# Kernel optimization log

Measured on AMD Instinct MI355X. Metric: run time of the kernel, lower is better.

The kernel has to match this reference:

```python
import jax, jax.numpy as jnp
import numpy as np

N_NODES = 50000
N_EDGES = 800000
IN_CH = 256
OUT_CH = 128


def setup_inputs() -> dict:
    key = jax.random.key(0)
    k1, k2, k3, k4, k5, k6 = jax.random.split(key, 6)
    x = jax.random.normal(k1, (N_NODES, IN_CH), dtype=jnp.float32)
    edge_rows = jax.random.randint(k2, (N_EDGES,), 0, N_NODES, dtype=jnp.int64)
    edge_cols = jax.random.randint(k3, (N_EDGES,), 0, N_NODES, dtype=jnp.int64)
    # positive edge weights, roughly like a normalized adjacency (~1/degree)
    edge_vals = jax.random.uniform(k4, (N_EDGES,), dtype=jnp.float32) / 16.0
    # xavier_uniform: bound = sqrt(6/(fan_in+fan_out))
    bound = float(np.sqrt(6.0 / (IN_CH + OUT_CH)))
    weight = jax.random.uniform(k5, (IN_CH, OUT_CH), dtype=jnp.float32, minval=-bound, maxval=bound)
    gate_weight = jax.random.uniform(k6, (IN_CH, OUT_CH), dtype=jnp.float32, minval=-bound, maxval=bound)
    return {"x": x, "edge_rows": edge_rows, "edge_cols": edge_cols,
            "edge_vals": edge_vals, "weight": weight, "gate_weight": gate_weight}


def _spmm(edge_rows, edge_cols, edge_vals, dense, n_rows):
    # out[r] = sum over edges (r, c, v): v * dense[c]
    gathered = edge_vals[:, None] * dense[edge_cols]  # [E, out_ch]
    return jax.ops.segment_sum(gathered, edge_rows, num_segments=n_rows)


def reference(x, edge_rows, edge_cols, edge_vals, weight, gate_weight):
    support = x @ weight          # [N, out_ch]
    gate = x @ gate_weight        # [N, out_ch]
    n = x.shape[0]
    agg_support = _spmm(edge_rows, edge_cols, edge_vals, support, n)
    agg_gate = _spmm(edge_rows, edge_cols, edge_vals, gate, n)
    return jax.nn.sigmoid(agg_gate) * agg_support
```

## Files before the change

### kernel.cpp

```cpp
#include <hip/hip_runtime.h>
#include <hip/hip_bf16.h>

#define IN_CH 256
#define OUT_CH 128
#define CAP 64
#define RPB 128
#define EPB 4096
#define NBIN 392
#define METAST 400

typedef __attribute__((ext_vector_type(8))) short bf16x8;
typedef __attribute__((ext_vector_type(4))) float f32x4;

__device__ __forceinline__ unsigned short f2bf(float f) {
  unsigned int u = __builtin_bit_cast(unsigned int, f);
  u += 0x7FFFu + ((u >> 16) & 1u);
  return (unsigned short)(u >> 16);
}
__device__ __forceinline__ unsigned int pack2bf(float a, float b) {
  return (unsigned int)f2bf(a) | ((unsigned int)f2bf(b) << 16);
}
__device__ __forceinline__ float bflo(unsigned int u) {
  return __builtin_bit_cast(float, u << 16);
}
__device__ __forceinline__ float bfhi(unsigned int u) {
  return __builtin_bit_cast(float, u & 0xFFFF0000u);
}

__global__ __launch_bounds__(256) void init_wcat(
    const float* __restrict__ w, const float* __restrict__ gw,
    unsigned short* __restrict__ wcat2) {
  const int c = blockIdx.x;
  const int k = threadIdx.x;
  const int wc = c >> 6, s = c & 63, n = s >> 4, lr = s & 15;
  const int ch = 32 * wc + (n & 1) * 16 + lr;
  const float v = (n < 2) ? w[(size_t)k * 128 + ch]
                          : gw[(size_t)k * 128 + ch];
  wcat2[(size_t)c * 256 + k] = f2bf(v);
}

#define AST 80

__global__ __launch_bounds__(256) void gemm_and_bin(
    const float* __restrict__ x, const unsigned short* __restrict__ wcat2,
    char* __restrict__ comb, int nrows,
    const int* __restrict__ er, const int* __restrict__ ec,
    const float* __restrict__ ev, uint2* __restrict__ seg,
    unsigned* __restrict__ meta, int E, int binBlocks) {
  __shared__ char smem[37728];

  if (blockIdx.x < binBlocks) {
    uint2* image = (uint2*)smem;
    int* hist = (int*)(smem + 32768);
    int* offs = (int*)(smem + 32768 + 1568);
    int* cur  = (int*)(smem + 32768 + 3136);
    int* gsum = (int*)(smem + 32768 + 4704);
    const int t = threadIdx.x;
    const int e0 = blockIdx.x * EPB;

    for (int j = t; j < NBIN; j += 256) hist[j] = 0;
    __syncthreads();

    int myr[16];
#pragma unroll
    for (int i = 0; i < 16; ++i) {
      const int e = e0 + i * 256 + t;
      int r = -1;
      if (e < E) { r = er[e]; atomicAdd(&hist[r >> 7], 1); }
      myr[i] = r;
    }
    __syncthreads();

    if (t < 49) {
      int s = 0;
#pragma unroll
      for (int k2 = 0; k2 < 8; ++k2) {
        const int j = t * 8 + k2;
        if (j < NBIN) { cur[j] = s; s += hist[j]; }
      }
      gsum[t] = s;
    }
    __syncthreads();
    if (t == 0) {
      int s = 0;
      for (int b2 = 0; b2 < 49; ++b2) { const int g = gsum[b2]; gsum[b2] = s; s += g; }
    }
    __syncthreads();
    if (t < 49) {
#pragma unroll
      for (int k2 = 0; k2 < 8; ++k2) {
        const int j = t * 8 + k2;
        if (j < NBIN) offs[j] = cur[j] + gsum[t];
      }
    }
    __syncthreads();
    for (int j = t; j < NBIN; j += 256) cur[j] = offs[j];
    __syncthreads();

#pragma unroll
    for (int i = 0; i < 16; ++i) {
      const int r = myr[i];
      if (r >= 0) {
        const int e = e0 + i * 256 + t;
        const int b2 = r >> 7;
        const int idx = atomicAdd(&cur[b2], 1);
        image[idx] = make_uint2(((unsigned)ec[e] << 16) | (unsigned)f2bf(ev[e]),
                                (unsigned)(r & (RPB - 1)));
      }
    }
    __syncthreads();

    uint2* segb = seg + (size_t)blockIdx.x * EPB;
    for (int s2 = t; s2 < EPB; s2 += 256) segb[s2] = image[s2];
    unsigned* metab = meta + (size_t)blockIdx.x * METAST;
    for (int j = t; j < NBIN - 1; j += 256)
      metab[j] = (unsigned)offs[j] | ((unsigned)hist[j] << 16);
    return;
  }

  char* As = smem;
  char* Bs = smem + 64 * AST;
  const int t = threadIdx.x;
  const int lane = t & 63;
  const int wc = t >> 6;
  const int lrow = lane & 15;
  const int klane = lane >> 4;
  const int blockRow = (blockIdx.x - binBlocks) * 64;

  f32x4 acc[4][4];
#pragma unroll
  for (int m = 0; m < 4; ++m)
#pragma unroll
    for (int n = 0; n < 4; ++n) acc[m][n] = (f32x4){0.f, 0.f, 0.f, 0.f};

  const int arow = t >> 2;
  const int aseg = t & 3;
  const int agrow = blockRow + arow;
  const bool aok = (agrow < nrows);
  const float* xrow = x + (size_t)agrow * IN_CH + aseg * 8;
  const char* bsrc0 = (const char*)wcat2 + (size_t)t * 512;

  for (int kt = 0; kt < IN_CH; kt += 32) {
    {
      float4 v0 = make_float4(0, 0, 0, 0), v1 = v0;
      if (aok) {
        v0 = *(const float4*)(xrow + kt);
        v1 = *(const float4*)(xrow + kt + 4);
      }
      uint4 pk;
      pk.x = pack2bf(v0.x, v0.y); pk.y = pack2bf(v0.z, v0.w);
      pk.z = pack2bf(v1.x, v1.y); pk.w = pack2bf(v1.z, v1.w);
      *(uint4*)(As + arow * AST + aseg * 16) = pk;
    }
    {
      const char* src = bsrc0 + kt * 2;
      char* dst = Bs + t * AST;
      *(uint4*)(dst + 0)  = *(const uint4*)(src + 0);
      *(uint4*)(dst + 16) = *(const uint4*)(src + 16);
      *(uint4*)(dst + 32) = *(const uint4*)(src + 32);
      *(uint4*)(dst + 48) = *(const uint4*)(src + 48);
    }
    __syncthreads();

    bf16x8 af[4], bfm[4];
#pragma unroll
    for (int m = 0; m < 4; ++m)
      af[m] = *(const bf16x8*)(As + (m * 16 + lrow) * AST + klane * 16);
#pragma unroll
    for (int n = 0; n < 4; ++n)
      bfm[n] = *(const bf16x8*)(Bs + (wc * 64 + n * 16 + lrow) * AST + klane * 16);
#pragma unroll
    for (int m = 0; m < 4; ++m)
#pragma unroll
      for (int n = 0; n < 4; ++n)
        acc[m][n] = __builtin_amdgcn_mfma_f32_16x16x32_bf16(af[m], bfm[n], acc[m][n], 0, 0, 0);
    __syncthreads();
  }

#pragma unroll
  for (int m = 0; m < 4; ++m) {
#pragma unroll
    for (int j = 0; j < 4; ++j) {
      const int grow = blockRow + m * 16 + klane * 4 + j;
      if (grow < nrows) {
        uint2 val;
        val.x = pack2bf(acc[m][0][j], acc[m][2][j]);
        val.y = pack2bf(acc[m][1][j], acc[m][3][j]);
        *(uint2*)(comb + (size_t)grow * 512 + wc * 128 + lrow * 8) = val;
      }
    }
  }
}

__global__ __launch_bounds__(256) void bin_fine2(
    const uint2* __restrict__ seg, const unsigned* __restrict__ meta,
    int* __restrict__ cnt, unsigned* __restrict__ bucket4,
    int nrows, int nblk) {
  __shared__ unsigned fine[RPB * CAP];
  __shared__ int lcnt[RPB];
  __shared__ int roff[224];
  __shared__ int S[224];
  __shared__ int Pex[225];
  const int t = threadIdx.x;
  const int j = blockIdx.x;
  const int r0 = j * RPB;

  for (int k = t; k < RPB; k += 256) lcnt[k] = 0;
  if (t < 224) {
    if (t < nblk) {
      const unsigned m = meta[(size_t)t * METAST + j];
      roff[t] = (int)(m & 0xFFFFu);
      S[t] = (int)(m >> 16);
    } else {
      S[t] = 0;
    }
  }
  __syncthreads();

  for (int d = 1; d < 224; d <<= 1) {
    int v = 0;
    if (t < 224 && t >= d) v = S[t - d];
    __syncthreads();
    if (t < 224) S[t] += v;
    __syncthreads();
  }
  if (t == 0) Pex[0] = 0;
  if (t < 224) Pex[t + 1] = S[t];
  __syncthreads();

  const int nE = Pex[nblk];
  for (int e = t; e < nE; e += 256) {
    int lo = 0, hi = nblk - 1;
    while (lo < hi) {
      const int mid = (lo + hi + 1) >> 1;
      if (Pex[mid] <= e) lo = mid; else hi = mid - 1;
    }
    const int i = e - Pex[lo];
    const uint2 ent = seg[(size_t)lo * EPB + roff[lo] + i];
    const int rl = (int)ent.y;
    const int idx = atomicAdd(&lcnt[rl], 1);
    if (idx < CAP) fine[rl * CAP + idx] = ent.x;
  }
  __syncthreads();

  if (t < RPB && r0 + t < nrows) cnt[r0 + t] = min(lcnt[t], CAP);

  for (int s = t; s < RPB * CAP; s += 256) {
    const int rl = s >> 6;
    const int sl = s & 63;
    if (sl < min(lcnt[rl], CAP) && r0 + rl < nrows)
      bucket4[(size_t)(r0 + rl) * CAP + sl] = fine[s];
  }
}

__global__ __launch_bounds__(256) void spmm_fused(
    const unsigned* __restrict__ bucket4, const int* __restrict__ cnt,
    const char* __restrict__ comb, float* __restrict__ out, int nrows) {
  const int wid = (int)((blockIdx.x * 256 + threadIdx.x) >> 6);
  const int lane = threadIdx.x & 63;
  if (wid >= nrows) return;

  const int deg = min(cnt[wid], CAP);
  float s1 = 0.f, g1 = 0.f, s2 = 0.f, g2 = 0.f;

  if (deg > 0) {
    const unsigned my = bucket4[(size_t)wid * CAP + lane];
    for (int d = 0; d < deg; d += 8) {
      unsigned cj[8]; float vj[8]; uint2 q[8];
#pragma unroll
      for (int j = 0; j < 8; ++j) {
        const int dj = d + j;
        const int ds = dj < deg ? dj : deg - 1;
        const unsigned ent = (unsigned)__shfl((int)my, ds);
        cj[j] = ent >> 16;
        vj[j] = (dj < deg) ? bflo(ent) : 0.f;
      }
#pragma unroll
      for (int j = 0; j < 8; ++j)
        q[j] = *(const uint2*)(comb + (size_t)cj[j] * 512 + lane * 8);
#pragma unroll
      for (int j = 0; j < 8; ++j) {
        s1 += vj[j] * bflo(q[j].x);  g1 += vj[j] * bfhi(q[j].x);
        s2 += vj[j] * bflo(q[j].y);  g2 += vj[j] * bfhi(q[j].y);
      }
    }
  }
  const int gg = lane >> 4, lr = lane & 15;
  const int c1 = 32 * gg + lr;
  const float o1 = s1 / (1.f + __expf(-g1));
  const float o2 = s2 / (1.f + __expf(-g2));
  out[(size_t)wid * OUT_CH + c1]      = o1;
  out[(size_t)wid * OUT_CH + c1 + 16] = o2;
}

extern "C" void kernel_launch(void* const* d_in, const int* in_sizes, int n_in,
                              void* d_out, int out_size, void* d_ws, size_t ws_size,
                              hipStream_t stream) {
  const float* x  = (const float*)d_in[0];
  const int*   er = (const int*)d_in[1];
  const int*   ec = (const int*)d_in[2];
  const float* ev = (const float*)d_in[3];
  const float* w  = (const float*)d_in[4];
  const float* gw = (const float*)d_in[5];
  float* out = (float*)d_out;

  const int N = in_sizes[0] / IN_CH;
  const int E = in_sizes[1];
  const int nbins = (N + RPB - 1) / RPB;
  const int binBlocks = (E + EPB - 1) / EPB;

  char* ws = (char*)d_ws;
  char* comb = ws;
  size_t off = (size_t)N * 512;
  unsigned short* wcat2 = (unsigned short*)(ws + off);  off += 256 * 256 * 2;
  int* cnt = (int*)(ws + off);                          off += ((size_t)N * 4 + 255) & ~255ull;
  unsigned* bucket4 = (unsigned*)(ws + off);            off += (size_t)N * CAP * 4;
  uint2* seg = (uint2*)(ws + off);                      off += (size_t)binBlocks * EPB * 8;
  unsigned* meta = (unsigned*)(ws + off);

  init_wcat<<<256, 256, 0, stream>>>(w, gw, wcat2);

  const int gemmBlocks = (N + 63) / 64;
  gemm_and_bin<<<binBlocks + gemmBlocks, 256, 0, stream>>>(
      x, wcat2, comb, N, er, ec, ev, seg, meta, E, binBlocks);

  bin_fine2<<<nbins, 256, 0, stream>>>(seg, meta, cnt, bucket4, N, binBlocks);

  const int blocks = (N + 3) / 4;
  spmm_fused<<<blocks, 256, 0, stream>>>(bucket4, cnt, comb, out, N);
}
```

Baseline: 105.3 us.

## Split x conversion from GEMM, fuse GEMM with fine binning, use LDS direct loads

A new first kernel converts x to bf16 in place inside the workspace while the coarse binning runs alongside it. The GEMM then moves into a 512-thread kernel that stages tiles with global_load_lds and shares its launch with the fine-binning blocks, so the old separate bin_fine2 launch is gone. The GEMM also writes its output over the bf16 x buffer it reads from. Coarse-bin entries are split into a 4-byte column/value array and a 1-byte row array to cut traffic, and the SpMM gather batch grows from 8 to 16 loads. Costs are an extra full pass over x in bf16 and a hazard: a GEMM block overwrites rows of combx that other blocks may still be reading, although each block reads only its own 128 rows.

```diff
diff --git a/kernel.cpp b/kernel.cpp
--- a/kernel.cpp
+++ b/kernel.cpp
@@ -25,6 +25,12 @@
 }
 __device__ __forceinline__ float bfhi(unsigned int u) {
   return __builtin_bit_cast(float, u & 0xFFFF0000u);
+}
+
+__device__ __forceinline__ void gl16(const void* g, void* l) {
+  __builtin_amdgcn_global_load_lds(
+      (const __attribute__((address_space(1))) void*)g,
+      (__attribute__((address_space(3))) void*)l, 16, 0, 0);
 }
 
 __global__ __launch_bounds__(256) void init_wcat(
@@ -39,173 +45,193 @@
   wcat2[(size_t)c * 256 + k] = f2bf(v);
 }
 
-#define AST 80
-
-__global__ __launch_bounds__(256) void gemm_and_bin(
-    const float* __restrict__ x, const unsigned short* __restrict__ wcat2,
-    char* __restrict__ comb, int nrows,
+__global__ __launch_bounds__(256) void cvt_and_bin(
+    const float* __restrict__ x, char* __restrict__ combx, int out16max,
     const int* __restrict__ er, const int* __restrict__ ec,
-    const float* __restrict__ ev, uint2* __restrict__ seg,
-    unsigned* __restrict__ meta, int E, int binBlocks) {
+    const float* __restrict__ ev, unsigned* __restrict__ cA,
+    unsigned* __restrict__ cB32, unsigned* __restrict__ meta,
+    int E, int nbins, int cvtBlocks) {
   __shared__ char smem[37728];
-
-  if (blockIdx.x < binBlocks) {
-    uint2* image = (uint2*)smem;
-    int* hist = (int*)(smem + 32768);
-    int* offs = (int*)(smem + 32768 + 1568);
-    int* cur  = (int*)(smem + 32768 + 3136);
-    int* gsum = (int*)(smem + 32768 + 4704);
-    const int t = threadIdx.x;
-    const int e0 = blockIdx.x * EPB;
-
-    for (int j = t; j < NBIN; j += 256) hist[j] = 0;
-    __syncthreads();
-
-    int myr[16];
-#pragma unroll
-    for (int i = 0; i < 16; ++i) {
+  const int t = threadIdx.x;
+
+  if ((int)blockIdx.x < cvtBlocks) {
+    const float4* x4 = (const float4*)x;
+    uint4* o16 = (uint4*)combx;
+    const size_t base = (size_t)blockIdx.x * 2048;
+#pragma unroll
+    for (int i = 0; i < 8; ++i) {
+      const size_t o = base + i * 256 + t;
+      if (o < (size_t)out16max) {
+        const float4 v0 = x4[o * 2];
+        const float4 v1 = x4[o * 2 + 1];
+        uint4 pk;
+        pk.x = pack2bf(v0.x, v0.y); pk.y = pack2bf(v0.z, v0.w);
+        pk.z = pack2bf(v1.x, v1.y); pk.w = pack2bf(v1.z, v1.w);
+        o16[o] = pk;
+      }
+    }
+    return;
+  }
+
+  uint2* image = (uint2*)smem;
+  int* hist = (int*)(smem + 32768);
+  int* offs = (int*)(smem + 32768 + 1568);
+  int* cur  = (int*)(smem + 32768 + 3136);
+  int* gsum = (int*)(smem + 32768 + 4704);
+  const int bb = blockIdx.x - cvtBlocks;
+  const int e0 = bb * EPB;
+
+  for (int j = t; j < NBIN; j += 256) hist[j] = 0;
+  __syncthreads();
+
+  int myr[16];
+#pragma unroll
+  for (int i = 0; i < 16; ++i) {
+    const int e = e0 + i * 256 + t;
+    int r = -1;
+    if (e < E) { r = er[e]; atomicAdd(&hist[r >> 7], 1); }
+    myr[i] = r;
+  }
+  __syncthreads();
+
+  if (t < 49) {
+    int s = 0;
+#pragma unroll
+    for (int k2 = 0; k2 < 8; ++k2) {
+      const int j = t * 8 + k2;
+      if (j < NBIN) { cur[j] = s; s += hist[j]; }
+    }
+    gsum[t] = s;
+  }
+  __syncthreads();
+  if (t == 0) {
+    int s = 0;
+    for (int b2 = 0; b2 < 49; ++b2) { const int g = gsum[b2]; gsum[b2] = s; s += g; }
+  }
+  __syncthreads();
+  if (t < 49) {
+#pragma unroll
+    for (int k2 = 0; k2 < 8; ++k2) {
+      const int j = t * 8 + k2;
+      if (j < NBIN) offs[j] = cur[j] + gsum[t];
+    }
+  }
+  __syncthreads();
+  for (int j = t; j < NBIN; j += 256) cur[j] = offs[j];
+  __syncthreads();
+
+#pragma unroll
+  for (int i = 0; i < 16; ++i) {
+    const int r = myr[i];
+    if (r >= 0) {
       const int e = e0 + i * 256 + t;
-      int r = -1;
-      if (e < E) { r = er[e]; atomicAdd(&hist[r >> 7], 1); }
-      myr[i] = r;
-    }
-    __syncthreads();
-
-    if (t < 49) {
-      int s = 0;
-#pragma unroll
-      for (int k2 = 0; k2 < 8; ++k2) {
-        const int j = t * 8 + k2;
-        if (j < NBIN) { cur[j] = s; s += hist[j]; }
-      }
-      gsum[t] = s;
-    }
-    __syncthreads();
-    if (t == 0) {
-      int s = 0;
-      for (int b2 = 0; b2 < 49; ++b2) { const int g = gsum[b2]; gsum[b2] = s; s += g; }
-    }
-    __syncthreads();
-    if (t < 49) {
-#pragma unroll
-      for (int k2 = 0; k2 < 8; ++k2) {
-        const int j = t * 8 + k2;
-        if (j < NBIN) offs[j] = cur[j] + gsum[t];
-      }
-    }
-    __syncthreads();
-    for (int j = t; j < NBIN; j += 256) cur[j] = offs[j];
-    __syncthreads();
-
-#pragma unroll
-    for (int i = 0; i < 16; ++i) {
-      const int r = myr[i];
-      if (r >= 0) {
-        const int e = e0 + i * 256 + t;
-        const int b2 = r >> 7;
-        const int idx = atomicAdd(&cur[b2], 1);
-        image[idx] = make_uint2(((unsigned)ec[e] << 16) | (unsigned)f2bf(ev[e]),
-                                (unsigned)(r & (RPB - 1)));
-      }
-    }
-    __syncthreads();
-
-    uint2* segb = seg + (size_t)blockIdx.x * EPB;
-    for (int s2 = t; s2 < EPB; s2 += 256) segb[s2] = image[s2];
-    unsigned* metab = meta + (size_t)blockIdx.x * METAST;
-    for (int j = t; j < NBIN - 1; j += 256)
-      metab[j] = (unsigned)offs[j] | ((unsigned)hist[j] << 16);
+      const int b2 = r >> 7;
+      const int idx = atomicAdd(&cur[b2], 1);
+      image[idx] = make_uint2(((unsigned)ec[e] << 16) | (unsigned)f2bf(ev[e]),
+                              (unsigned)(r & (RPB - 1)));
+    }
+  }
+  __syncthreads();
+
+  unsigned* cAb = cA + (size_t)bb * EPB;
+  for (int s2 = t; s2 < EPB; s2 += 256) cAb[s2] = image[s2].x;
+  unsigned* cBb = cB32 + (size_t)bb * (EPB / 4);
+  for (int s2 = t; s2 < EPB / 4; s2 += 256) {
+    cBb[s2] = (image[4 * s2].y) | (image[4 * s2 + 1].y << 8) |
+              (image[4 * s2 + 2].y << 16) | (image[4 * s2 + 3].y << 24);
+  }
+  unsigned* metab = meta + (size_t)bb * METAST;
+  for (int j = t; j < nbins; j += 256)
+    metab[j] = (unsigned)offs[j] | ((unsigned)hist[j] << 16);
+}
+
+__global__ __launch_bounds__(512) void gemm_and_fine(
+    char* __restrict__ combx, const unsigned short* __restrict__ wcat2,
+    int nrows, const unsigned* __restrict__ cA, const unsigned* __restrict__ cB32,
+    const unsigned* __restrict__ meta, int* __restrict__ cnt,
+    unsigned* __restrict__ bucket4, int nblk, int gemmBlocks) {
+  __shared__ char smem[49152];
+  const int t = threadIdx.x;
+
+  if ((int)blockIdx.x < gemmBlocks) {
+    char* As = smem;
+    char* Bs = smem + 16384;
+    const int lane = t & 63;
+    const int wv = t >> 6;
+    const int wr = wv >> 2;
+    const int wc = wv & 3;
+    const int lrow = lane & 15;
+    const int klane = lane >> 4;
+    const int blockRow = blockIdx.x * 128;
+
+    f32x4 acc[4][4];
+#pragma unroll
+    for (int m = 0; m < 4; ++m)
+#pragma unroll
+      for (int n = 0; n < 4; ++n) acc[m][n] = (f32x4){0.f, 0.f, 0.f, 0.f};
+
+    const char* wb = (const char*)wcat2;
+
+    for (int kt = 0; kt < 4; ++kt) {
+      const int kb = kt * 128;
+#pragma unroll
+      for (int r = 0; r < 2; ++r) {
+        const int L = t + r * 512;
+        const int row = L >> 3, kc = L & 7;
+        gl16(combx + (size_t)(blockRow + row) * 512 + kb + kc * 16, As + L * 16);
+      }
+#pragma unroll
+      for (int r = 0; r < 4; ++r) {
+        const int L = t + r * 512;
+        const int cp = L >> 3, kc = L & 7;
+        gl16(wb + (size_t)cp * 512 + kb + kc * 16, Bs + L * 16);
+      }
+      __syncthreads();
+
+#pragma unroll
+      for (int kk = 0; kk < 2; ++kk) {
+        bf16x8 af[4], bfm[4];
+#pragma unroll
+        for (int m = 0; m < 4; ++m)
+          af[m] = *(const bf16x8*)(As + (wr * 64 + m * 16 + lrow) * 128 + kk * 64 + klane * 16);
+#pragma unroll
+        for (int n = 0; n < 4; ++n)
+          bfm[n] = *(const bf16x8*)(Bs + (wc * 64 + n * 16 + lrow) * 128 + kk * 64 + klane * 16);
+#pragma unroll
+        for (int m = 0; m < 4; ++m)
+#pragma unroll
+          for (int n = 0; n < 4; ++n)
+            acc[m][n] = __builtin_amdgcn_mfma_f32_16x16x32_bf16(af[m], bfm[n], acc[m][n], 0, 0, 0);
+      }
+      __syncthreads();
+    }
+
+#pragma unroll
+    for (int m = 0; m < 4; ++m) {
+#pragma unroll
+      for (int j = 0; j < 4; ++j) {
+        const int grow = blockRow + wr * 64 + m * 16 + klane * 4 + j;
+        if (grow < nrows) {
+          uint2 val;
+          val.x = pack2bf(acc[m][0][j], acc[m][2][j]);
+          val.y = pack2bf(acc[m][1][j], acc[m][3][j]);
+          *(uint2*)(combx + (size_t)grow * 512 + wc * 128 + lrow * 8) = val;
+        }
+      }
+    }
     return;
   }
 
-  char* As = smem;
-  char* Bs = smem + 64 * AST;
-  const int t = threadIdx.x;
-  const int lane = t & 63;
-  const int wc = t >> 6;
-  const int lrow = lane & 15;
-  const int klane = lane >> 4;
-  const int blockRow = (blockIdx.x - binBlocks) * 64;
-
-  f32x4 acc[4][4];
-#pragma unroll
-  for (int m = 0; m < 4; ++m)
-#pragma unroll
-    for (int n = 0; n < 4; ++n) acc[m][n] = (f32x4){0.f, 0.f, 0.f, 0.f};
-
-  const int arow = t >> 2;
-  const int aseg = t & 3;
-  const int agrow = blockRow + arow;
-  const bool aok = (agrow < nrows);
-  const float* xrow = x + (size_t)agrow * IN_CH + aseg * 8;
-  const char* bsrc0 = (const char*)wcat2 + (size_t)t * 512;
-
-  for (int kt = 0; kt < IN_CH; kt += 32) {
-    {
-      float4 v0 = make_float4(0, 0, 0, 0), v1 = v0;
-      if (aok) {
-        v0 = *(const float4*)(xrow + kt);
-        v1 = *(const float4*)(xrow + kt + 4);
-      }
-      uint4 pk;
-      pk.x = pack2bf(v0.x, v0.y); pk.y = pack2bf(v0.z, v0.w);
-      pk.z = pack2bf(v1.x, v1.y); pk.w = pack2bf(v1.z, v1.w);
-      *(uint4*)(As + arow * AST + aseg * 16) = pk;
-    }
-    {
-      const char* src = bsrc0 + kt * 2;
-      char* dst = Bs + t * AST;
-      *(uint4*)(dst + 0)  = *(const uint4*)(src + 0);
-      *(uint4*)(dst + 16) = *(const uint4*)(src + 16);
-      *(uint4*)(dst + 32) = *(const uint4*)(src + 32);
-      *(uint4*)(dst + 48) = *(const uint4*)(src + 48);
-    }
-    __syncthreads();
-
-    bf16x8 af[4], bfm[4];
-#pragma unroll
-    for (int m = 0; m < 4; ++m)
-      af[m] = *(const bf16x8*)(As + (m * 16 + lrow) * AST + klane * 16);
-#pragma unroll
-    for (int n = 0; n < 4; ++n)
-      bfm[n] = *(const bf16x8*)(Bs + (wc * 64 + n * 16 + lrow) * AST + klane * 16);
-#pragma unroll
-    for (int m = 0; m < 4; ++m)
-#pragma unroll
-      for (int n = 0; n < 4; ++n)
-        acc[m][n] = __builtin_amdgcn_mfma_f32_16x16x32_bf16(af[m], bfm[n], acc[m][n], 0, 0, 0);
-    __syncthreads();
-  }
-
-#pragma unroll
-  for (int m = 0; m < 4; ++m) {
-#pragma unroll
-    for (int j = 0; j < 4; ++j) {
-      const int grow = blockRow + m * 16 + klane * 4 + j;
-      if (grow < nrows) {
-        uint2 val;
-        val.x = pack2bf(acc[m][0][j], acc[m][2][j]);
-        val.y = pack2bf(acc[m][1][j], acc[m][3][j]);
-        *(uint2*)(comb + (size_t)grow * 512 + wc * 128 + lrow * 8) = val;
-      }
-    }
-  }
-}
-
-__global__ __launch_bounds__(256) void bin_fine2(
-    const uint2* __restrict__ seg, const unsigned* __restrict__ meta,
-    int* __restrict__ cnt, unsigned* __restrict__ bucket4,
-    int nrows, int nblk) {
-  __shared__ unsigned fine[RPB * CAP];
-  __shared__ int lcnt[RPB];
-  __shared__ int roff[224];
-  __shared__ int S[224];
-  __shared__ int Pex[225];
-  const int t = threadIdx.x;
-  const int j = blockIdx.x;
+  unsigned* fine = (unsigned*)smem;
+  int* lcnt = (int*)(smem + 32768);
+  int* roff = (int*)(smem + 32768 + 512);
+  int* S    = (int*)(smem + 32768 + 512 + 896);
+  int* Pex  = (int*)(smem + 32768 + 512 + 1792);
+  const int j = blockIdx.x - gemmBlocks;
   const int r0 = j * RPB;
-
-  for (int k = t; k < RPB; k += 256) lcnt[k] = 0;
+  const unsigned char* cB8 = (const unsigned char*)cB32;
+
+  for (int k = t; k < RPB; k += 512) lcnt[k] = 0;
   if (t < 224) {
     if (t < nblk) {
       const unsigned m = meta[(size_t)t * METAST + j];
@@ -229,23 +255,23 @@
   __syncthreads();
 
   const int nE = Pex[nblk];
-  for (int e = t; e < nE; e += 256) {
+  for (int e = t; e < nE; e += 512) {
     int lo = 0, hi = nblk - 1;
     while (lo < hi) {
       const int mid = (lo + hi + 1) >> 1;
       if (Pex[mid] <= e) lo = mid; else hi = mid - 1;
     }
     const int i = e - Pex[lo];
-    const uint2 ent = seg[(size_t)lo * EPB + roff[lo] + i];
-    const int rl = (int)ent.y;
+    const unsigned a = cA[(size_t)lo * EPB + roff[lo] + i];
+    const int rl = (int)cB8[(size_t)lo * EPB + roff[lo] + i];
     const int idx = atomicAdd(&lcnt[rl], 1);
-    if (idx < CAP) fine[rl * CAP + idx] = ent.x;
+    if (idx < CAP) fine[rl * CAP + idx] = a;
   }
   __syncthreads();
 
   if (t < RPB && r0 + t < nrows) cnt[r0 + t] = min(lcnt[t], CAP);
 
-  for (int s = t; s < RPB * CAP; s += 256) {
+  for (int s = t; s < RPB * CAP; s += 512) {
     const int rl = s >> 6;
     const int sl = s & 63;
     if (sl < min(lcnt[rl], CAP) && r0 + rl < nrows)
@@ -265,10 +291,10 @@
 
   if (deg > 0) {
     const unsigned my = bucket4[(size_t)wid * CAP + lane];
-    for (int d = 0; d < deg; d += 8) {
-      unsigned cj[8]; float vj[8]; uint2 q[8];
-#pragma unroll
-      for (int j = 0; j < 8; ++j) {
+    for (int d = 0; d < deg; d += 16) {
+      unsigned cj[16]; float vj[16]; uint2 q[16];
+#pragma unroll
+      for (int j = 0; j < 16; ++j) {
         const int dj = d + j;
         const int ds = dj < deg ? dj : deg - 1;
         const unsigned ent = (unsigned)__shfl((int)my, ds);
@@ -276,10 +302,10 @@
         vj[j] = (dj < deg) ? bflo(ent) : 0.f;
       }
 #pragma unroll
-      for (int j = 0; j < 8; ++j)
+      for (int j = 0; j < 16; ++j)
         q[j] = *(const uint2*)(comb + (size_t)cj[j] * 512 + lane * 8);
 #pragma unroll
-      for (int j = 0; j < 8; ++j) {
+      for (int j = 0; j < 16; ++j) {
         s1 += vj[j] * bflo(q[j].x);  g1 += vj[j] * bfhi(q[j].x);
         s2 += vj[j] * bflo(q[j].y);  g2 += vj[j] * bfhi(q[j].y);
       }
@@ -308,24 +334,29 @@
   const int E = in_sizes[1];
   const int nbins = (N + RPB - 1) / RPB;
   const int binBlocks = (E + EPB - 1) / EPB;
+  const int gemmBlocks = (N + 127) / 128;
+  const int Npad = gemmBlocks * 128;
 
   char* ws = (char*)d_ws;
-  char* comb = ws;
-  size_t off = (size_t)N * 512;
+  char* combx = ws;
+  size_t off = (size_t)Npad * 512;
   unsigned short* wcat2 = (unsigned short*)(ws + off);  off += 256 * 256 * 2;
   int* cnt = (int*)(ws + off);                          off += ((size_t)N * 4 + 255) & ~255ull;
   unsigned* bucket4 = (unsigned*)(ws + off);            off += (size_t)N * CAP * 4;
-  uint2* seg = (uint2*)(ws + off);                      off += (size_t)binBlocks * EPB * 8;
+  unsigned* cA = (unsigned*)(ws + off);                 off += (size_t)binBlocks * EPB * 4;
+  unsigned* cB32 = (unsigned*)(ws + off);               off += (size_t)binBlocks * EPB;
   unsigned* meta = (unsigned*)(ws + off);
 
   init_wcat<<<256, 256, 0, stream>>>(w, gw, wcat2);
 
-  const int gemmBlocks = (N + 63) / 64;
-  gemm_and_bin<<<binBlocks + gemmBlocks, 256, 0, stream>>>(
-      x, wcat2, comb, N, er, ec, ev, seg, meta, E, binBlocks);
-
-  bin_fine2<<<nbins, 256, 0, stream>>>(seg, meta, cnt, bucket4, N, binBlocks);
+  const int out16max = N * 32;
+  const int cvtBlocks = (out16max + 2047) / 2048;
+  cvt_and_bin<<<cvtBlocks + binBlocks, 256, 0, stream>>>(
+      x, combx, out16max, er, ec, ev, cA, cB32, meta, E, nbins, cvtBlocks);
+
+  gemm_and_fine<<<gemmBlocks + nbins, 512, 0, stream>>>(
+      combx, wcat2, N, cA, cB32, meta, cnt, bucket4, binBlocks, gemmBlocks);
 
   const int blocks = (N + 3) / 4;
-  spmm_fused<<<blocks, 256, 0, stream>>>(bucket4, cnt, comb, out, N);
-}
+  spmm_fused<<<blocks, 256, 0, stream>>>(bucket4, cnt, combx, out, N);
+}
```

Result: slower. 121.6 us (+15.5%).

## Fuse fine binning and SpMM gather into one per-bin kernel

Applied to the files above, without the earlier changes.

Merges the fine-binning kernel and the SpMM kernel so each 512-thread block bins its 128 rows into shared memory and then gathers and applies the gated sigmoid directly from LDS. This removes the global bucket/count buffers and their write/read round trip plus one kernel launch. In exchange, the SpMM phase now runs with far fewer, larger blocks (one per 128-row bin), lowering the number of waves available to hide gather latency.

```diff
diff --git a/kernel.cpp b/kernel.cpp
--- a/kernel.cpp
+++ b/kernel.cpp
@@ -46,7 +46,7 @@
     char* __restrict__ comb, int nrows,
     const int* __restrict__ er, const int* __restrict__ ec,
     const float* __restrict__ ev, uint2* __restrict__ seg,
-    unsigned* __restrict__ meta, int E, int binBlocks) {
+    unsigned* __restrict__ meta, int E, int nbins, int binBlocks) {
   __shared__ char smem[37728];
 
   if (blockIdx.x < binBlocks) {
@@ -113,7 +113,7 @@
     uint2* segb = seg + (size_t)blockIdx.x * EPB;
     for (int s2 = t; s2 < EPB; s2 += 256) segb[s2] = image[s2];
     unsigned* metab = meta + (size_t)blockIdx.x * METAST;
-    for (int j = t; j < NBIN - 1; j += 256)
+    for (int j = t; j < nbins; j += 256)
       metab[j] = (unsigned)offs[j] | ((unsigned)hist[j] << 16);
     return;
   }
@@ -192,9 +192,9 @@
   }
 }
 
-__global__ __launch_bounds__(256) void bin_fine2(
+__global__ __launch_bounds__(512) void spmm_mega(
     const uint2* __restrict__ seg, const unsigned* __restrict__ meta,
-    int* __restrict__ cnt, unsigned* __restrict__ bucket4,
+    const char* __restrict__ comb, float* __restrict__ out,
     int nrows, int nblk) {
   __shared__ unsigned fine[RPB * CAP];
   __shared__ int lcnt[RPB];
@@ -205,7 +205,7 @@
   const int j = blockIdx.x;
   const int r0 = j * RPB;
 
-  for (int k = t; k < RPB; k += 256) lcnt[k] = 0;
+  if (t < RPB) lcnt[t] = 0;
   if (t < 224) {
     if (t < nblk) {
       const unsigned m = meta[(size_t)t * METAST + j];
@@ -229,7 +229,7 @@
   __syncthreads();
 
   const int nE = Pex[nblk];
-  for (int e = t; e < nE; e += 256) {
+  for (int e = t; e < nE; e += 512) {
     int lo = 0, hi = nblk - 1;
     while (lo < hi) {
       const int mid = (lo + hi + 1) >> 1;
@@ -243,54 +243,46 @@
   }
   __syncthreads();
 
-  if (t < RPB && r0 + t < nrows) cnt[r0 + t] = min(lcnt[t], CAP);
-
-  for (int s = t; s < RPB * CAP; s += 256) {
-    const int rl = s >> 6;
-    const int sl = s & 63;
-    if (sl < min(lcnt[rl], CAP) && r0 + rl < nrows)
-      bucket4[(size_t)(r0 + rl) * CAP + sl] = fine[s];
-  }
-}
-
-__global__ __launch_bounds__(256) void spmm_fused(
-    const unsigned* __restrict__ bucket4, const int* __restrict__ cnt,
-    const char* __restrict__ comb, float* __restrict__ out, int nrows) {
-  const int wid = (int)((blockIdx.x * 256 + threadIdx.x) >> 6);
-  const int lane = threadIdx.x & 63;
-  if (wid >= nrows) return;
-
-  const int deg = min(cnt[wid], CAP);
-  float s1 = 0.f, g1 = 0.f, s2 = 0.f, g2 = 0.f;
-
-  if (deg > 0) {
-    const unsigned my = bucket4[(size_t)wid * CAP + lane];
-    for (int d = 0; d < deg; d += 8) {
-      unsigned cj[8]; float vj[8]; uint2 q[8];
-#pragma unroll
-      for (int j = 0; j < 8; ++j) {
-        const int dj = d + j;
-        const int ds = dj < deg ? dj : deg - 1;
-        const unsigned ent = (unsigned)__shfl((int)my, ds);
-        cj[j] = ent >> 16;
-        vj[j] = (dj < deg) ? bflo(ent) : 0.f;
-      }
-#pragma unroll
-      for (int j = 0; j < 8; ++j)
-        q[j] = *(const uint2*)(comb + (size_t)cj[j] * 512 + lane * 8);
-#pragma unroll
-      for (int j = 0; j < 8; ++j) {
-        s1 += vj[j] * bflo(q[j].x);  g1 += vj[j] * bfhi(q[j].x);
-        s2 += vj[j] * bflo(q[j].y);  g2 += vj[j] * bfhi(q[j].y);
-      }
-    }
-  }
+  const int w = t >> 6;
+  const int lane = t & 63;
   const int gg = lane >> 4, lr = lane & 15;
   const int c1 = 32 * gg + lr;
-  const float o1 = s1 / (1.f + __expf(-g1));
-  const float o2 = s2 / (1.f + __expf(-g2));
-  out[(size_t)wid * OUT_CH + c1]      = o1;
-  out[(size_t)wid * OUT_CH + c1 + 16] = o2;
+
+  for (int i = 0; i < 16; ++i) {
+    const int rl = w * 16 + i;
+    const int wid = r0 + rl;
+    const int deg = min(lcnt[rl], CAP);
+    float s1 = 0.f, g1 = 0.f, s2 = 0.f, g2 = 0.f;
+
+    if (deg > 0) {
+      const unsigned my = fine[rl * CAP + lane];
+      for (int d = 0; d < deg; d += 8) {
+        unsigned cj[8]; float vj[8]; uint2 q[8];
+#pragma unroll
+        for (int k = 0; k < 8; ++k) {
+          const int dk = d + k;
+          const int ds = dk < deg ? dk : deg - 1;
+          const unsigned ent = (unsigned)__shfl((int)my, ds);
+          cj[k] = ent >> 16;
+          vj[k] = (dk < deg) ? bflo(ent) : 0.f;
+        }
+#pragma unroll
+        for (int k = 0; k < 8; ++k)
+          q[k] = *(const uint2*)(comb + (size_t)cj[k] * 512 + lane * 8);
+#pragma unroll
+        for (int k = 0; k < 8; ++k) {
+          s1 += vj[k] * bflo(q[k].x);  g1 += vj[k] * bfhi(q[k].x);
+          s2 += vj[k] * bflo(q[k].y);  g2 += vj[k] * bfhi(q[k].y);
+        }
+      }
+    }
+    if (wid < nrows) {
+      const float o1 = s1 / (1.f + __expf(-g1));
+      const float o2 = s2 / (1.f + __expf(-g2));
+      out[(size_t)wid * OUT_CH + c1]      = o1;
+      out[(size_t)wid * OUT_CH + c1 + 16] = o2;
+    }
+  }
 }
 
 extern "C" void kernel_launch(void* const* d_in, const int* in_sizes, int n_in,
@@ -313,8 +305,6 @@
   char* comb = ws;
   size_t off = (size_t)N * 512;
   unsigned short* wcat2 = (unsigned short*)(ws + off);  off += 256 * 256 * 2;
-  int* cnt = (int*)(ws + off);                          off += ((size_t)N * 4 + 255) & ~255ull;
-  unsigned* bucket4 = (unsigned*)(ws + off);            off += (size_t)N * CAP * 4;
   uint2* seg = (uint2*)(ws + off);                      off += (size_t)binBlocks * EPB * 8;
   unsigned* meta = (unsigned*)(ws + off);
 
@@ -322,10 +312,7 @@
 
   const int gemmBlocks = (N + 63) / 64;
   gemm_and_bin<<<binBlocks + gemmBlocks, 256, 0, stream>>>(
-      x, wcat2, comb, N, er, ec, ev, seg, meta, E, binBlocks);
-
-  bin_fine2<<<nbins, 256, 0, stream>>>(seg, meta, cnt, bucket4, N, binBlocks);
-
-  const int blocks = (N + 3) / 4;
-  spmm_fused<<<blocks, 256, 0, stream>>>(bucket4, cnt, comb, out, N);
-}
+      x, wcat2, comb, N, er, ec, ev, seg, meta, E, nbins, binBlocks);
+
+  spmm_mega<<<nbins, 512, 0, stream>>>(seg, meta, comb, out, N, binBlocks);
+}
```

Result: faster. 101.3 us (-3.8%).
